# Kernel tuning notes

Measured on AMD Instinct MI355X. Metric: run time of the kernel, lower is better.

Reference implementation:

```python
import jax, jax.numpy as jnp
import numpy as np

D_G, D_2D, D_3D = 512, 768, 1024
D_F, RANK, ATTN_H = 256, 16, 512
B = 8192


def _xavier(key, shape):
    fan_out, fan_in = shape
    lim = float(np.sqrt(6.0 / (fan_in + fan_out)))
    return jax.random.uniform(key, shape, jnp.float32, -lim, lim)


def setup_inputs() -> dict:
    key = jax.random.key(0)
    ks = jax.random.split(key, 12)
    inp = {
        "h_g": jax.random.normal(ks[0], (B, D_G), jnp.float32),
        "h_2d": jax.random.normal(ks[1], (B, D_2D), jnp.float32),
        "h_3d": jax.random.normal(ks[2], (B, D_3D), jnp.float32),
        # modality projections (torch Linear: y = x @ W.T + b)
        "Wg": _xavier(ks[3], (D_F, D_G)),   "bg": jnp.zeros((D_F,), jnp.float32),
        "W2": _xavier(ks[4], (D_F, D_2D)),  "b2": jnp.zeros((D_F,), jnp.float32),
        "W3": _xavier(ks[5], (D_F, D_3D)),  "b3": jnp.zeros((D_F,), jnp.float32),
        # LayerNorm affine params
        "ln_g_w": jnp.ones((D_F,), jnp.float32),  "ln_g_b": jnp.zeros((D_F,), jnp.float32),
        "ln_2_w": jnp.ones((D_F,), jnp.float32),  "ln_2_b": jnp.zeros((D_F,), jnp.float32),
        "ln_3_w": jnp.ones((D_F,), jnp.float32),  "ln_3_b": jnp.zeros((D_F,), jnp.float32),
        # rank expansions (no bias)
        "U": _xavier(ks[6], (RANK * D_F, D_F)),
        "V": _xavier(ks[7], (RANK * D_F, D_F)),
        "S": _xavier(ks[8], (RANK * D_F, D_F)),
        # attention MLP
        "Wa1": _xavier(ks[9], (ATTN_H, D_G + D_2D + D_3D)), "ba1": jnp.zeros((ATTN_H,), jnp.float32),
        "Wa2": _xavier(ks[10], (RANK, ATTN_H)),             "ba2": jnp.zeros((RANK,), jnp.float32),
    }
    return inp


def _layernorm(x, w, b, eps=1e-5):
    mu = jnp.mean(x, axis=-1, keepdims=True)
    var = jnp.var(x, axis=-1, keepdims=True)
    return (x - mu) * jax.lax.rsqrt(var + eps) * w + b


def reference(h_g, h_2d, h_3d, Wg, bg, W2, b2, W3, b3,
              ln_g_w, ln_g_b, ln_2_w, ln_2_b, ln_3_w, ln_3_b,
              U, V, S, Wa1, ba1, Wa2, ba2):
    # proj + LN + ReLU (dropout=0 / eval mode)
    g = jax.nn.relu(_layernorm(h_g @ Wg.T + bg, ln_g_w, ln_g_b))
    d2 = jax.nn.relu(_layernorm(h_2d @ W2.T + b2, ln_2_w, ln_2_b))
    d3 = jax.nn.relu(_layernorm(h_3d @ W3.T + b3, ln_3_w, ln_3_b))
    b = g.shape[0]
    # rank expansion: (B, R, d_f)
    g_r = (g @ U.T).reshape(b, RANK, D_F)
    d2_r = (d2 @ V.T).reshape(b, RANK, D_F)
    d3_r = (d3 @ S.T).reshape(b, RANK, D_F)
    z_r = g_r * d2_r * d3_r  # elementwise tri-linear product
    # rank attention from raw modality concat
    h_cat = jnp.concatenate([h_g, h_2d, h_3d], axis=-1)
    beta = jax.nn.softmax(jax.nn.relu(h_cat @ Wa1.T + ba1) @ Wa2.T + ba2, axis=-1)  # (B, R)
    z = jnp.einsum('brd,br->bd', z_r, beta)  # (B, d_f)
    return z
```

## Files before the change

### kernel.cpp

```cpp
#include <hip/hip_runtime.h>
#include <stdint.h>

#define B_ROWS 8192
#define DG 512
#define D2 768
#define D3 1024
#define DCAT 2304
#define DF 256
#define RANK 16
#define AH 512

#define OFF_WG 0
#define OFF_W2 131072
#define OFF_W3 327680
#define OFF_U  589824
#define OFF_V  1638400
#define OFF_S  2686976
#define OFF_WA1 3735552

#define WS_WBUF  0u
#define WS_HG    9830400u
#define WS_H2    18219008u
#define WS_H3    30801920u
#define WS_GBUF  9830400u
#define WS_PROJ  47579136u
#define WS_A1P   72744960u
#define WS_BETA  89522176u
#define WS_ZPART 47579136u
#define WS_REQUIRED 94240768u

typedef __attribute__((ext_vector_type(8))) short short8;
typedef __attribute__((ext_vector_type(4))) float f32x4;

__device__ inline unsigned short f2bf(float f) {
  union { float f; unsigned int u; } v; v.f = f;
  unsigned int u = v.u + 0x7fffu + ((v.u >> 16) & 1u);
  return (unsigned short)(u >> 16);
}
__device__ inline float bf2f(unsigned short h) {
  union { float f; unsigned int u; } v; v.u = ((unsigned int)h) << 16;
  return v.f;
}

typedef const unsigned int __attribute__((address_space(1)))* as1_u32p;
typedef unsigned int __attribute__((address_space(3)))* as3_u32p;

__device__ inline void g2l16(const unsigned short* g, unsigned short* l) {
  __builtin_amdgcn_global_load_lds((as1_u32p)g, (as3_u32p)l, 16, 0, 0);
}


__global__ __launch_bounds__(256) void cvt_split_k(const float* __restrict__ hg,
                                                   const float* __restrict__ h2,
                                                   const float* __restrict__ h3,
                                                   const float* __restrict__ Wg,
                                                   const float* __restrict__ W2,
                                                   const float* __restrict__ W3,
                                                   const float* __restrict__ U,
                                                   const float* __restrict__ V,
                                                   const float* __restrict__ S,
                                                   const float* __restrict__ Wa1,
                                                   unsigned short* __restrict__ hgb,
                                                   unsigned short* __restrict__ h2b,
                                                   unsigned short* __restrict__ h3b,
                                                   unsigned short* __restrict__ wbuf) {
  const int bid = blockIdx.x;
  const float* src;
  unsigned short* dst;
  int e;
  if (bid < 18432) {
    e = (bid * 256 + threadIdx.x) * 4;
    if (e < 4194304)        { src = hg + e;            dst = hgb + e; }
    else if (e < 10485760)  { src = h2 + (e - 4194304); dst = h2b + (e - 4194304); }
    else                    { src = h3 + (e - 10485760); dst = h3b + (e - 10485760); }
  } else {
    e = ((bid - 18432) * 256 + threadIdx.x) * 4;
    dst = wbuf + e;
    if (e < OFF_W2)       src = Wg  + e;
    else if (e < OFF_W3)  src = W2  + (e - OFF_W2);
    else if (e < OFF_U)   src = W3  + (e - OFF_W3);
    else if (e < OFF_V)   src = U   + (e - OFF_U);
    else if (e < OFF_S)   src = V   + (e - OFF_V);
    else if (e < OFF_WA1) src = S   + (e - OFF_S);
    else                  src = Wa1 + (e - OFF_WA1);
  }
  float4 v = *(const float4*)src;
  ushort4 o;
  o.x = f2bf(v.x); o.y = f2bf(v.y); o.z = f2bf(v.z); o.w = f2bf(v.w);
  *(ushort4*)dst = o;
}


__device__ __forceinline__ void gemm_mainloop_acc(const unsigned short* Ag, int lda,
                                                  const unsigned short* Bg, int ldb,
                                                  int K,
                                                  unsigned short* lA, unsigned short* lB,
                                                  f32x4 acc[4][4]) {
  const int tid = threadIdx.x;
  const int lane = tid & 63;
  const int wr = tid >> 7;
  const int wc = (tid >> 6) & 1;
  const int row_s = tid >> 3;
  const int kc_s = (((tid & 7) ^ ((tid >> 3) & 7)) << 3);
  const int mbase = wr * 64 + (lane & 15);
  const int nbase = wc * 64 + (lane & 15);
  const int kq = lane >> 4;
  const int h = lane & 7;

  const int nsteps = K >> 6;
  for (int ks = 0; ks < nsteps; ++ks) {
    const int k0 = ks << 6;
    __syncthreads();
#pragma unroll
    for (int p = 0; p < 4; ++p) {
      const int row = p * 32 + row_s;
      const int lofs = (p * 256 + tid) * 8;
      g2l16(Ag + (size_t)row * lda + k0 + kc_s, lA + lofs);
      g2l16(Bg + (size_t)row * ldb + k0 + kc_s, lB + lofs);
    }
    __syncthreads();
#pragma unroll
    for (int kk = 0; kk < 2; ++kk) {
      const int kch = (kk << 2) + kq;
      const int ko = ((kch ^ h) << 3);
      short8 af[4], bfr[4];
#pragma unroll
      for (int t = 0; t < 4; ++t) {
        af[t]  = *(const short8*)(lA + (mbase + t * 16) * 64 + ko);
        bfr[t] = *(const short8*)(lB + (nbase + t * 16) * 64 + ko);
      }
#pragma unroll
      for (int ti = 0; ti < 4; ++ti)
#pragma unroll
        for (int tj = 0; tj < 4; ++tj)
          acc[ti][tj] = __builtin_amdgcn_mfma_f32_16x16x32_bf16(af[ti], bfr[tj], acc[ti][tj], 0, 0, 0);
    }
  }
}

__device__ __forceinline__ void zero_acc(f32x4 acc[4][4]) {
#pragma unroll
  for (int i = 0; i < 4; ++i)
#pragma unroll
    for (int j = 0; j < 4; ++j)
      acc[i][j] = (f32x4){0.f, 0.f, 0.f, 0.f};
}


__device__ __forceinline__ void gemm_mainloop_bk128(const unsigned short* Ag, int lda,
                                                    const unsigned short* Bg, int ldb,
                                                    int K,
                                                    unsigned short* lA, unsigned short* lB,
                                                    f32x4 acc[4][4]) {
  const int tid = threadIdx.x;
  const int lane = tid & 63;
  const int wr = tid >> 7;
  const int wc = (tid >> 6) & 1;
#pragma unroll
  for (int i = 0; i < 4; ++i)
#pragma unroll
    for (int j = 0; j < 4; ++j)
      acc[i][j] = (f32x4){0.f, 0.f, 0.f, 0.f};

  const int row_s = tid >> 4;
  const int kc_s = (((tid & 15) ^ ((tid >> 4) & 15)) << 3);
  const int mbase = wr * 64 + (lane & 15);
  const int nbase = wc * 64 + (lane & 15);
  const int kq = lane >> 4;
  const int h = lane & 15;

  const int nsteps = K >> 7;
  for (int ks = 0; ks < nsteps; ++ks) {
    const int k0 = ks << 7;
    __syncthreads();
#pragma unroll
    for (int p = 0; p < 8; ++p) {
      const int row = p * 16 + row_s;
      const int lofs = (p * 256 + tid) * 8;
      g2l16(Ag + (size_t)row * lda + k0 + kc_s, lA + lofs);
      g2l16(Bg + (size_t)row * ldb + k0 + kc_s, lB + lofs);
    }
    __syncthreads();
#pragma unroll
    for (int kk = 0; kk < 4; ++kk) {
      const int kch = (kk << 2) + kq;
      const int ko = ((kch ^ h) << 3);
      short8 af[4], bfr[4];
#pragma unroll
      for (int t = 0; t < 4; ++t) {
        af[t]  = *(const short8*)(lA + (mbase + t * 16) * 128 + ko);
        bfr[t] = *(const short8*)(lB + (nbase + t * 16) * 128 + ko);
      }
#pragma unroll
      for (int ti = 0; ti < 4; ++ti)
#pragma unroll
        for (int tj = 0; tj < 4; ++tj)
          acc[ti][tj] = __builtin_amdgcn_mfma_f32_16x16x32_bf16(af[ti], bfr[tj], acc[ti][tj], 0, 0, 0);
    }
  }
}


__global__ __launch_bounds__(256) void fatgemm_k(const unsigned short* __restrict__ hgb,
                                                 const unsigned short* __restrict__ h2b,
                                                 const unsigned short* __restrict__ h3b,
                                                 const unsigned short* __restrict__ wbuf,
                                                 float* __restrict__ proj,
                                                 unsigned short* __restrict__ a1part) {
  __shared__ __align__(16) unsigned short lA[128 * 64];
  __shared__ __align__(16) unsigned short lB[128 * 64];
  const int bid = blockIdx.x;
  f32x4 acc[4][4];
  const int lane = threadIdx.x & 63;
  const int wr = threadIdx.x >> 7, wc = (threadIdx.x >> 6) & 1;
  zero_acc(acc);

  if (bid < 384) {
    const int z = bid >> 7;
    const int local = bid & 127;
    const int m0 = (local >> 1) << 7;
    const int n0 = (local & 1) << 7;
    const int Kz   = (z == 0) ? DG : (z == 1 ? D2 : D3);
    const unsigned short* Ab = (z == 0) ? hgb : (z == 1 ? h2b : h3b);
    const int woff = (z == 0) ? OFF_WG : (z == 1 ? OFF_W2 : OFF_W3);
    gemm_mainloop_acc(Ab + (size_t)m0 * Kz, Kz,
                      wbuf + woff + (size_t)n0 * Kz, Kz, Kz, lA, lB, acc);
    float* out = proj + (size_t)z * B_ROWS * DF;
    const int r0 = m0 + wr * 64 + ((lane >> 4) << 2);
    const int c0 = n0 + wc * 64 + (lane & 15);
#pragma unroll
    for (int ti = 0; ti < 4; ++ti)
#pragma unroll
      for (int tj = 0; tj < 4; ++tj)
#pragma unroll
        for (int i = 0; i < 4; ++i)
          out[(size_t)(r0 + ti * 16 + i) * DF + (c0 + tj * 16)] = acc[ti][tj][i];
  } else {
    const int t = bid - 384;
    const int half = t >> 8;
    const int local = t & 255;
    const int m0 = (local >> 2) << 7;
    const int n0 = (local & 3) << 7;
    const unsigned short* Bb = wbuf + OFF_WA1 + (size_t)n0 * DCAT;
    if (half == 0) {
      gemm_mainloop_acc(hgb + (size_t)m0 * DG, DG, Bb, DCAT, DG, lA, lB, acc);
      gemm_mainloop_acc(h2b + (size_t)m0 * D2, D2, Bb + DG, DCAT, D2, lA, lB, acc);
    } else {
      gemm_mainloop_acc(h3b + (size_t)m0 * D3, D3, Bb + DG + D2, DCAT, D3, lA, lB, acc);
    }
    unsigned short* out = a1part + (size_t)half * (B_ROWS * AH);
    const int r0 = m0 + wr * 64 + ((lane >> 4) << 2);
    const int c0 = n0 + wc * 64 + (lane & 15);
#pragma unroll
    for (int ti = 0; ti < 4; ++ti)
#pragma unroll
      for (int tj = 0; tj < 4; ++tj)
#pragma unroll
        for (int i = 0; i < 4; ++i)
          out[(size_t)(r0 + ti * 16 + i) * AH + (c0 + tj * 16)] = f2bf(acc[ti][tj][i]);
  }
}


__global__ __launch_bounds__(256) void rank_fused_k(const unsigned short* __restrict__ gbuf,
                                                    const unsigned short* __restrict__ wbuf,
                                                    const float* __restrict__ beta,
                                                    float* __restrict__ zpart) {
  __shared__ __align__(16) unsigned short lA[128 * 128];
  __shared__ __align__(16) unsigned short lB[128 * 128];
  __shared__ float lbeta[4 * 128];
  const int m0 = blockIdx.x * 128;
  const int d0 = blockIdx.y * 128;
  const int rg = blockIdx.z * 4;

  for (int i = threadIdx.x; i < 512; i += 256) {
    const int rr = i >> 7, row = i & 127;
    lbeta[i] = beta[(size_t)(m0 + row) * RANK + rg + rr];
  }

  const int lane = threadIdx.x & 63;
  const int wr = threadIdx.x >> 7, wc = (threadIdx.x >> 6) & 1;
  const int lr0 = wr * 64 + ((lane >> 4) << 2);

  f32x4 zacc[4][4];
#pragma unroll
  for (int ti = 0; ti < 4; ++ti)
#pragma unroll
    for (int tj = 0; tj < 4; ++tj)
      zacc[ti][tj] = (f32x4){0.f, 0.f, 0.f, 0.f};

  for (int rr = 0; rr < 4; ++rr) {
    const int n0 = (rg + rr) * 256 + d0;
    f32x4 prod[4][4];
    f32x4 acc[4][4];
#pragma unroll
    for (int zi = 0; zi < 3; ++zi) {
      gemm_mainloop_bk128(gbuf + (size_t)zi * B_ROWS * DF + (size_t)m0 * DF, DF,
                          wbuf + OFF_U + (size_t)zi * 1048576 + (size_t)n0 * DF, DF, DF,
                          lA, lB, acc);
      if (zi == 0) {
#pragma unroll
        for (int ti = 0; ti < 4; ++ti)
#pragma unroll
          for (int tj = 0; tj < 4; ++tj)
            prod[ti][tj] = acc[ti][tj];
      } else {
#pragma unroll
        for (int ti = 0; ti < 4; ++ti)
#pragma unroll
          for (int tj = 0; tj < 4; ++tj)
            prod[ti][tj] *= acc[ti][tj];
      }
    }
#pragma unroll
    for (int ti = 0; ti < 4; ++ti) {
      const float4 b4 = *(const float4*)(lbeta + rr * 128 + lr0 + ti * 16);
      const float bv[4] = {b4.x, b4.y, b4.z, b4.w};
#pragma unroll
      for (int tj = 0; tj < 4; ++tj)
#pragma unroll
        for (int i = 0; i < 4; ++i)
          zacc[ti][tj][i] += prod[ti][tj][i] * bv[i];
    }
  }

  float* zp = zpart + (size_t)blockIdx.z * (B_ROWS * DF);
  const int c0 = d0 + wc * 64 + (lane & 15);
#pragma unroll
  for (int ti = 0; ti < 4; ++ti)
#pragma unroll
    for (int tj = 0; tj < 4; ++tj)
#pragma unroll
      for (int i = 0; i < 4; ++i)
        zp[(size_t)(m0 + lr0 + ti * 16 + i) * DF + (c0 + tj * 16)] = zacc[ti][tj][i];
}


__global__ __launch_bounds__(256) void zsum_k(const float* __restrict__ zpart,
                                              float* __restrict__ z) {
  const int idx = blockIdx.x * 256 + threadIdx.x;
  const size_t e = (size_t)idx * 4;
  const size_t stride = (size_t)B_ROWS * DF;
  float4 a = *(const float4*)(zpart + e);
  float4 b = *(const float4*)(zpart + stride + e);
  float4 c = *(const float4*)(zpart + 2 * stride + e);
  float4 d = *(const float4*)(zpart + 3 * stride + e);
  float4 o;
  o.x = (a.x + b.x) + (c.x + d.x);
  o.y = (a.y + b.y) + (c.y + d.y);
  o.z = (a.z + b.z) + (c.z + d.z);
  o.w = (a.w + b.w) + (c.w + d.w);
  *(float4*)(z + e) = o;
}


__global__ __launch_bounds__(256) void post_k(const float* __restrict__ proj,
                                              const float* __restrict__ bg, const float* __restrict__ b2, const float* __restrict__ b3,
                                              const float* __restrict__ wg, const float* __restrict__ wbg,
                                              const float* __restrict__ w2, const float* __restrict__ wb2,
                                              const float* __restrict__ w3, const float* __restrict__ wb3,
                                              unsigned short* __restrict__ gout,
                                              const unsigned short* __restrict__ a1part,
                                              const float* __restrict__ ba1,
                                              const float* __restrict__ Wa2,
                                              const float* __restrict__ ba2,
                                              float* __restrict__ beta) {
  const int bid = blockIdx.x;
  if (bid < 6144) {
    const int gid = bid * 4 + (threadIdx.x >> 6);
    const int lane = threadIdx.x & 63;
    const int z = gid >> 13;
    const int row = gid & (B_ROWS - 1);
    const float* bias = z == 0 ? bg : (z == 1 ? b2 : b3);
    const float* lw = z == 0 ? wg : (z == 1 ? w2 : w3);
    const float* lb = z == 0 ? wbg : (z == 1 ? wb2 : wb3);
    const float* x = proj + (size_t)z * B_ROWS * DF + (size_t)row * DF + lane * 4;
    float4 v = *(const float4*)x;
    float4 bb = *(const float4*)(bias + lane * 4);
    v.x += bb.x; v.y += bb.y; v.z += bb.z; v.w += bb.w;
    float s = v.x + v.y + v.z + v.w;
    float q = v.x * v.x + v.y * v.y + v.z * v.z + v.w * v.w;
#pragma unroll
    for (int m = 1; m < 64; m <<= 1) { s += __shfl_xor(s, m, 64); q += __shfl_xor(q, m, 64); }
    const float mean = s * (1.f / DF);
    const float var = q * (1.f / DF) - mean * mean;
    const float rs = rsqrtf(var + 1e-5f);
    float4 w4 = *(const float4*)(lw + lane * 4);
    float4 b4 = *(const float4*)(lb + lane * 4);
    ushort4 o;
    o.x = f2bf(fmaxf((v.x - mean) * rs * w4.x + b4.x, 0.f));
    o.y = f2bf(fmaxf((v.y - mean) * rs * w4.y + b4.y, 0.f));
    o.z = f2bf(fmaxf((v.z - mean) * rs * w4.z + b4.z, 0.f));
    o.w = f2bf(fmaxf((v.w - mean) * rs * w4.w + b4.w, 0.f));
    *(ushort4*)(gout + (size_t)z * B_ROWS * DF + (size_t)row * DF + lane * 4) = o;
  } else {
    __shared__ float lw[RANK * AH];
    for (int i = threadIdx.x; i < RANK * AH / 4; i += 256)
      *(float4*)(lw + i * 4) = *(const float4*)(Wa2 + i * 4);
    __syncthreads();
    const int row = (bid - 6144) * 4 + (threadIdx.x >> 6);
    const int lane = threadIdx.x & 63;
    const unsigned short* h0 = a1part + (size_t)row * AH + lane * 8;
    const unsigned short* h1 = h0 + (size_t)B_ROWS * AH;
    const uint4 p0 = *(const uint4*)h0;
    const uint4 p1 = *(const uint4*)h1;
    const unsigned int u0[4] = {p0.x, p0.y, p0.z, p0.w};
    const unsigned int u1[4] = {p1.x, p1.y, p1.z, p1.w};
    float4 ca = *(const float4*)(ba1 + lane * 8);
    float4 cb = *(const float4*)(ba1 + lane * 8 + 4);
    const float bias[8] = {ca.x, ca.y, ca.z, ca.w, cb.x, cb.y, cb.z, cb.w};
    float av[8];
#pragma unroll
    for (int j = 0; j < 4; ++j) {
      const float s0 = bf2f((unsigned short)(u0[j] & 0xffffu)) + bf2f((unsigned short)(u1[j] & 0xffffu));
      const float s1 = bf2f((unsigned short)(u0[j] >> 16)) + bf2f((unsigned short)(u1[j] >> 16));
      av[2 * j]     = fmaxf(s0 + bias[2 * j], 0.f);
      av[2 * j + 1] = fmaxf(s1 + bias[2 * j + 1], 0.f);
    }
    float lg[RANK];
#pragma unroll
    for (int r = 0; r < RANK; ++r) {
      const float* wrow = lw + r * AH + lane * 8;
      float4 wa = *(const float4*)wrow;
      float4 wb = *(const float4*)(wrow + 4);
      float p = av[0] * wa.x + av[1] * wa.y + av[2] * wa.z + av[3] * wa.w
              + av[4] * wb.x + av[5] * wb.y + av[6] * wb.z + av[7] * wb.w;
#pragma unroll
      for (int m = 1; m < 64; m <<= 1) p += __shfl_xor(p, m, 64);
      lg[r] = p + ba2[r];
    }
    float mx = lg[0];
#pragma unroll
    for (int r = 1; r < RANK; ++r) mx = fmaxf(mx, lg[r]);
    float den = 0.f;
#pragma unroll
    for (int r = 0; r < RANK; ++r) { lg[r] = __expf(lg[r] - mx); den += lg[r]; }
    const float inv = 1.f / den;
    if (lane < RANK) {
      float mine = 0.f;
#pragma unroll
      for (int r = 0; r < RANK; ++r) mine = (lane == r) ? lg[r] : mine;
      beta[(size_t)row * RANK + lane] = mine * inv;
    }
  }
}


extern "C" void kernel_launch(void* const* d_in, const int* in_sizes, int n_in,
                              void* d_out, int out_size, void* d_ws, size_t ws_size,
                              hipStream_t stream) {
  if (ws_size < (size_t)WS_REQUIRED) return;

  const float* h_g   = (const float*)d_in[0];
  const float* h_2d  = (const float*)d_in[1];
  const float* h_3d  = (const float*)d_in[2];
  const float* Wg    = (const float*)d_in[3];
  const float* bg    = (const float*)d_in[4];
  const float* W2    = (const float*)d_in[5];
  const float* b2    = (const float*)d_in[6];
  const float* W3    = (const float*)d_in[7];
  const float* b3    = (const float*)d_in[8];
  const float* ln_g_w = (const float*)d_in[9];
  const float* ln_g_b = (const float*)d_in[10];
  const float* ln_2_w = (const float*)d_in[11];
  const float* ln_2_b = (const float*)d_in[12];
  const float* ln_3_w = (const float*)d_in[13];
  const float* ln_3_b = (const float*)d_in[14];
  const float* U     = (const float*)d_in[15];
  const float* V     = (const float*)d_in[16];
  const float* S     = (const float*)d_in[17];
  const float* Wa1   = (const float*)d_in[18];
  const float* ba1   = (const float*)d_in[19];
  const float* Wa2   = (const float*)d_in[20];
  const float* ba2   = (const float*)d_in[21];

  char* ws = (char*)d_ws;
  unsigned short* wbuf   = (unsigned short*)(ws + WS_WBUF);
  unsigned short* hgb    = (unsigned short*)(ws + WS_HG);
  unsigned short* h2b    = (unsigned short*)(ws + WS_H2);
  unsigned short* h3b    = (unsigned short*)(ws + WS_H3);
  unsigned short* gbuf   = (unsigned short*)(ws + WS_GBUF);
  float*          proj   = (float*)(ws + WS_PROJ);
  unsigned short* a1part = (unsigned short*)(ws + WS_A1P);
  float*          beta   = (float*)(ws + WS_BETA);
  float*          zpart  = (float*)(ws + WS_ZPART);
  float* z = (float*)d_out;

  cvt_split_k<<<dim3(23232), dim3(256), 0, stream>>>(h_g, h_2d, h_3d,
                                                     Wg, W2, W3, U, V, S, Wa1,
                                                     hgb, h2b, h3b, wbuf);
  fatgemm_k<<<dim3(896), dim3(256), 0, stream>>>(hgb, h2b, h3b, wbuf, proj, a1part);
  post_k<<<dim3(8192), dim3(256), 0, stream>>>(proj, bg, b2, b3, ln_g_w, ln_g_b,
                                               ln_2_w, ln_2_b, ln_3_w, ln_3_b, gbuf,
                                               a1part, ba1, Wa2, ba2, beta);
  rank_fused_k<<<dim3(64, 2, 4), dim3(256), 0, stream>>>(gbuf, wbuf, beta, zpart);
  zsum_k<<<dim3(2048), dim3(256), 0, stream>>>(zpart, z);
}
```

Before: 322.9 us.

## Double-buffer LDS in rank_fused_k to overlap global loads with MFMA

Replaces the per-GEMM mainloop in rank_fused_k with a flattened 12-phase loop over rank and modality that double-buffers the A/B tiles in shared memory. The next K-chunk is issued into one buffer while the MFMAs consume the other, so global-to-LDS load latency can be hidden behind compute. The cost is doubled LDS use (about 128KB per block), which can reduce occupancy, plus more live accumulator registers.

```diff
diff --git a/kernel.cpp b/kernel.cpp
--- a/kernel.cpp
+++ b/kernel.cpp
@@ -147,60 +147,6 @@
 }
 
 
-__device__ __forceinline__ void gemm_mainloop_bk128(const unsigned short* Ag, int lda,
-                                                    const unsigned short* Bg, int ldb,
-                                                    int K,
-                                                    unsigned short* lA, unsigned short* lB,
-                                                    f32x4 acc[4][4]) {
-  const int tid = threadIdx.x;
-  const int lane = tid & 63;
-  const int wr = tid >> 7;
-  const int wc = (tid >> 6) & 1;
-#pragma unroll
-  for (int i = 0; i < 4; ++i)
-#pragma unroll
-    for (int j = 0; j < 4; ++j)
-      acc[i][j] = (f32x4){0.f, 0.f, 0.f, 0.f};
-
-  const int row_s = tid >> 4;
-  const int kc_s = (((tid & 15) ^ ((tid >> 4) & 15)) << 3);
-  const int mbase = wr * 64 + (lane & 15);
-  const int nbase = wc * 64 + (lane & 15);
-  const int kq = lane >> 4;
-  const int h = lane & 15;
-
-  const int nsteps = K >> 7;
-  for (int ks = 0; ks < nsteps; ++ks) {
-    const int k0 = ks << 7;
-    __syncthreads();
-#pragma unroll
-    for (int p = 0; p < 8; ++p) {
-      const int row = p * 16 + row_s;
-      const int lofs = (p * 256 + tid) * 8;
-      g2l16(Ag + (size_t)row * lda + k0 + kc_s, lA + lofs);
-      g2l16(Bg + (size_t)row * ldb + k0 + kc_s, lB + lofs);
-    }
-    __syncthreads();
-#pragma unroll
-    for (int kk = 0; kk < 4; ++kk) {
-      const int kch = (kk << 2) + kq;
-      const int ko = ((kch ^ h) << 3);
-      short8 af[4], bfr[4];
-#pragma unroll
-      for (int t = 0; t < 4; ++t) {
-        af[t]  = *(const short8*)(lA + (mbase + t * 16) * 128 + ko);
-        bfr[t] = *(const short8*)(lB + (nbase + t * 16) * 128 + ko);
-      }
-#pragma unroll
-      for (int ti = 0; ti < 4; ++ti)
-#pragma unroll
-        for (int tj = 0; tj < 4; ++tj)
-          acc[ti][tj] = __builtin_amdgcn_mfma_f32_16x16x32_bf16(af[ti], bfr[tj], acc[ti][tj], 0, 0, 0);
-    }
-  }
-}
-
-
 __global__ __launch_bounds__(256) void fatgemm_k(const unsigned short* __restrict__ hgb,
                                                  const unsigned short* __restrict__ h2b,
                                                  const unsigned short* __restrict__ h3b,
@@ -266,62 +212,114 @@
                                                     const unsigned short* __restrict__ wbuf,
                                                     const float* __restrict__ beta,
                                                     float* __restrict__ zpart) {
-  __shared__ __align__(16) unsigned short lA[128 * 128];
-  __shared__ __align__(16) unsigned short lB[128 * 128];
+  __shared__ __align__(16) unsigned short lA[2 * 128 * 128];
+  __shared__ __align__(16) unsigned short lB[2 * 128 * 128];
   __shared__ float lbeta[4 * 128];
   const int m0 = blockIdx.x * 128;
   const int d0 = blockIdx.y * 128;
   const int rg = blockIdx.z * 4;
-
-  for (int i = threadIdx.x; i < 512; i += 256) {
+  const int tid = threadIdx.x;
+
+  for (int i = tid; i < 512; i += 256) {
     const int rr = i >> 7, row = i & 127;
     lbeta[i] = beta[(size_t)(m0 + row) * RANK + rg + rr];
   }
 
-  const int lane = threadIdx.x & 63;
-  const int wr = threadIdx.x >> 7, wc = (threadIdx.x >> 6) & 1;
+  const int lane = tid & 63;
+  const int wr = tid >> 7, wc = (tid >> 6) & 1;
+  const int row_s = tid >> 4;
+  const int kc_s = (((tid & 15) ^ ((tid >> 4) & 15)) << 3);
+  const int mbase = wr * 64 + (lane & 15);
+  const int nbase = wc * 64 + (lane & 15);
+  const int kq = lane >> 4;
+  const int h = lane & 15;
   const int lr0 = wr * 64 + ((lane >> 4) << 2);
 
-  f32x4 zacc[4][4];
+  auto stage = [&](int rr, int zi, int ks, unsigned short* dA, unsigned short* dB) {
+    const unsigned short* Ag = gbuf + (size_t)zi * (B_ROWS * DF) + (size_t)m0 * DF + (ks << 7);
+    const unsigned short* Bg = wbuf + OFF_U + (size_t)zi * 1048576
+                             + (size_t)((rg + rr) * 256 + d0) * DF + (ks << 7);
+#pragma unroll
+    for (int q = 0; q < 8; ++q) {
+      const int row = q * 16 + row_s;
+      const int lofs = (q * 256 + tid) * 8;
+      g2l16(Ag + (size_t)row * DF + kc_s, dA + lofs);
+      g2l16(Bg + (size_t)row * DF + kc_s, dB + lofs);
+    }
+  };
+
+  f32x4 zacc[4][4], prod[4][4], acc[4][4];
 #pragma unroll
   for (int ti = 0; ti < 4; ++ti)
 #pragma unroll
-    for (int tj = 0; tj < 4; ++tj)
+    for (int tj = 0; tj < 4; ++tj) {
       zacc[ti][tj] = (f32x4){0.f, 0.f, 0.f, 0.f};
-
-  for (int rr = 0; rr < 4; ++rr) {
-    const int n0 = (rg + rr) * 256 + d0;
-    f32x4 prod[4][4];
-    f32x4 acc[4][4];
-#pragma unroll
-    for (int zi = 0; zi < 3; ++zi) {
-      gemm_mainloop_bk128(gbuf + (size_t)zi * B_ROWS * DF + (size_t)m0 * DF, DF,
-                          wbuf + OFF_U + (size_t)zi * 1048576 + (size_t)n0 * DF, DF, DF,
-                          lA, lB, acc);
-      if (zi == 0) {
-#pragma unroll
-        for (int ti = 0; ti < 4; ++ti)
-#pragma unroll
-          for (int tj = 0; tj < 4; ++tj)
-            prod[ti][tj] = acc[ti][tj];
-      } else {
-#pragma unroll
-        for (int ti = 0; ti < 4; ++ti)
-#pragma unroll
-          for (int tj = 0; tj < 4; ++tj)
-            prod[ti][tj] *= acc[ti][tj];
+      acc[ti][tj]  = (f32x4){0.f, 0.f, 0.f, 0.f};
+    }
+
+  auto compute = [&](const unsigned short* sA, const unsigned short* sB) {
+#pragma unroll
+    for (int kk = 0; kk < 4; ++kk) {
+      const int kch = (kk << 2) + kq;
+      const int ko = ((kch ^ h) << 3);
+      short8 af[4], bfr[4];
+#pragma unroll
+      for (int t = 0; t < 4; ++t) {
+        af[t]  = *(const short8*)(sA + (mbase + t * 16) * 128 + ko);
+        bfr[t] = *(const short8*)(sB + (nbase + t * 16) * 128 + ko);
       }
-    }
-#pragma unroll
-    for (int ti = 0; ti < 4; ++ti) {
-      const float4 b4 = *(const float4*)(lbeta + rr * 128 + lr0 + ti * 16);
-      const float bv[4] = {b4.x, b4.y, b4.z, b4.w};
+#pragma unroll
+      for (int ti = 0; ti < 4; ++ti)
+#pragma unroll
+        for (int tj = 0; tj < 4; ++tj)
+          acc[ti][tj] = __builtin_amdgcn_mfma_f32_16x16x32_bf16(af[ti], bfr[tj], acc[ti][tj], 0, 0, 0);
+    }
+  };
+
+  stage(0, 0, 0, lA, lB);
+  for (int p = 0; p < 12; ++p) {
+    const int rr = p / 3;
+    const int zi = p - rr * 3;
+    __syncthreads();
+    stage(rr, zi, 1, lA + 16384, lB + 16384);
+    compute(lA, lB);
+    __syncthreads();
+    if (p + 1 < 12) {
+      const int pn = p + 1;
+      const int rrn = pn / 3;
+      stage(rrn, pn - rrn * 3, 0, lA, lB);
+    }
+    compute(lA + 16384, lB + 16384);
+
+    if (zi == 0) {
+#pragma unroll
+      for (int ti = 0; ti < 4; ++ti)
+#pragma unroll
+        for (int tj = 0; tj < 4; ++tj)
+          prod[ti][tj] = acc[ti][tj];
+    } else if (zi == 1) {
+#pragma unroll
+      for (int ti = 0; ti < 4; ++ti)
+#pragma unroll
+        for (int tj = 0; tj < 4; ++tj)
+          prod[ti][tj] *= acc[ti][tj];
+    } else {
+#pragma unroll
+      for (int ti = 0; ti < 4; ++ti) {
+        const float4 b4 = *(const float4*)(lbeta + rr * 128 + lr0 + ti * 16);
+        const float bv[4] = {b4.x, b4.y, b4.z, b4.w};
+#pragma unroll
+        for (int tj = 0; tj < 4; ++tj)
+#pragma unroll
+          for (int i = 0; i < 4; ++i)
+            zacc[ti][tj][i] += prod[ti][tj][i] * acc[ti][tj][i] * bv[i];
+      }
+    }
+#pragma unroll
+    for (int ti = 0; ti < 4; ++ti)
 #pragma unroll
       for (int tj = 0; tj < 4; ++tj)
-#pragma unroll
-        for (int i = 0; i < 4; ++i)
-          zacc[ti][tj][i] += prod[ti][tj][i] * bv[i];
-    }
+        acc[ti][tj] = (f32x4){0.f, 0.f, 0.f, 0.f};
   }
 
   float* zp = zpart + (size_t)blockIdx.z * (B_ROWS * DF);
```

New measurement: 323.4 us. Within noise of the previous version (+0.2%).
